# Kernel tuning notes

Hardware: AMD Instinct MI355X
Metric: run time of the kernel (lower is better)

The kernel has to match this reference:

```python
import jax, jax.numpy as jnp
import numpy as np

B, S, E, H = 1, 2048, 512, 8
D = E // H
N = B * S
WIN_HALF = 32  # attention_window 64 -> +/-32
ALPHA = 0.1
LN_EPS = 1e-12
NEG_INF = -1e9


def _build_window_edges():
    # windowed graph: dst i attends to src j with |i-j| <= WIN_HALF, within each batch block
    i = np.arange(S)
    offs = np.arange(-WIN_HALF, WIN_HALF + 1)
    src = i[:, None] + offs[None, :]
    dst = np.broadcast_to(i[:, None], src.shape)
    valid = (src >= 0) & (src < S)
    src, dst = src[valid], dst[valid]
    srcs, dsts = [], []
    for b in range(B):
        srcs.append(src + b * S)
        dsts.append(dst + b * S)
    return (np.concatenate(srcs).astype(np.int32),
            np.concatenate(dsts).astype(np.int32))


def setup_inputs() -> dict:
    key = jax.random.key(0)
    ks = jax.random.split(key, 12)
    sc = 1.0 / np.sqrt(E)
    src_np, dst_np = _build_window_edges()
    return {
        "hidden_states": jax.random.normal(ks[0], (B, S, E), dtype=jnp.float32),
        "attention_mask": jnp.zeros((B, S), dtype=jnp.float32),
        "edge_src": jnp.asarray(src_np),
        "edge_dst": jnp.asarray(dst_np),
        "Wq": jax.random.normal(ks[1], (E, E), dtype=jnp.float32) * sc,
        "bq": jnp.zeros((E,), dtype=jnp.float32),
        "Wk": jax.random.normal(ks[2], (E, E), dtype=jnp.float32) * sc,
        "bk": jnp.zeros((E,), dtype=jnp.float32),
        "Wv": jax.random.normal(ks[3], (E, E), dtype=jnp.float32) * sc,
        "bv": jnp.zeros((E,), dtype=jnp.float32),
        "Wo": jax.random.normal(ks[4], (E, E), dtype=jnp.float32) * sc,
        "bo": jnp.zeros((E,), dtype=jnp.float32),
        "ln_g": jnp.ones((E,), dtype=jnp.float32),
        "ln_b": jnp.zeros((E,), dtype=jnp.float32),
    }


def reference(hidden_states, attention_mask, edge_src, edge_dst,
              Wq, bq, Wk, bk, Wv, bv, Wo, bo, ln_g, ln_b):
    x = hidden_states  # (B,S,E); node ordering n = b*S + s (matches torch reshape)
    q = ((x @ Wq + bq) / jnp.sqrt(jnp.asarray(D, x.dtype))).reshape(N, H, D)
    k = (x @ Wk + bk).reshape(N, H, D)
    v = (x @ Wv + bv).reshape(N, H, D)

    mask = (attention_mask >= 0).reshape(N)  # bool per node

    # u_dot_v('k','q','score'): per-edge, per-head dot product
    score = jnp.einsum('ehd,ehd->eh', k[edge_src], q[edge_dst])  # (Eg,H)
    score = jnp.where(mask[edge_src][:, None], score, NEG_INF)

    # edge_softmax over incoming edges of each destination node
    smax = jax.ops.segment_max(score, edge_dst, num_segments=N)
    p = jnp.exp(score - smax[edge_dst])
    denom = jax.ops.segment_sum(p, edge_dst, num_segments=N)
    p = p / denom[edge_dst]  # (Eg,H)

    # 5 diffusion steps: h <- A h, blended with residual v (dropout off in eval)
    h = v
    for _ in range(5):
        m = h[edge_src] * p[:, :, None]                      # u_mul_e
        h = jax.ops.segment_sum(m, edge_dst, num_segments=N)  # sum('m','h')
        h = (1.0 - ALPHA) * h + ALPHA * v

    attn = h.reshape(B, S, E)

    # DiffuserSelfOutput: dense -> residual add -> LayerNorm
    y = attn @ Wo + bo + hidden_states
    mu = y.mean(-1, keepdims=True)
    var = ((y - mu) ** 2).mean(-1, keepdims=True)
    out = (y - mu) * jax.lax.rsqrt(var + LN_EPS) * ln_g + ln_b
    return out
```

## Files before the change

### kernel.cpp

```cpp
#include <hip/hip_runtime.h>
#include <math.h>

#define S_LEN 2048
#define E_DIM 512
#define NE (S_LEN * E_DIM)
#define H_NUM 8
#define WH 32
#define NOFF 65
#define PROW (H_NUM * NOFF)
#define PN (S_LEN * PROW)

typedef float f32x4 __attribute__((ext_vector_type(4)));
typedef short short8 __attribute__((ext_vector_type(8)));

__device__ __forceinline__ unsigned short f2bf(float f) {
    union { float f; unsigned u; } cv; cv.f = f;
    unsigned u = cv.u;
    u += 0x7fffu + ((u >> 16) & 1u);
    return (unsigned short)(u >> 16);
}
__device__ __forceinline__ unsigned pk2(float x, float y) {
    return (unsigned)f2bf(x) | ((unsigned)f2bf(y) << 16);
}

__device__ __forceinline__ void mfma_gemm_f32(
    const float* __restrict__ A, const float* __restrict__ W,
    const float* __restrict__ bias, float* __restrict__ C,
    float scale, int m0, int n0)
{
    __shared__ unsigned short As[64 * 40];
    __shared__ unsigned short Bs[64 * 40];
    const int tid = threadIdx.x;
    const int lane = tid & 63, wave = tid >> 6;
    const int quad = lane >> 4, l16 = lane & 15;
    const int wr = (wave >> 1) * 32, wc = (wave & 1) * 32;
    const int ar = tid >> 2, ac = (tid & 3) * 8;
    const int bn = tid & 63, bk0 = (tid >> 6) * 8;

    f32x4 acc00 = {0.f,0.f,0.f,0.f}, acc01 = acc00, acc10 = acc00, acc11 = acc00;

    for (int kk = 0; kk < E_DIM; kk += 32) {
        float4 a0 = *(const float4*)(A + (size_t)(m0 + ar) * E_DIM + kk + ac);
        float4 a1 = *(const float4*)(A + (size_t)(m0 + ar) * E_DIM + kk + ac + 4);
        float b[8];
#pragma unroll
        for (int j = 0; j < 8; ++j)
            b[j] = W[(size_t)(kk + bk0 + j) * E_DIM + n0 + bn];
        __syncthreads();
        uint4 ap; ap.x = pk2(a0.x, a0.y); ap.y = pk2(a0.z, a0.w);
        ap.z = pk2(a1.x, a1.y); ap.w = pk2(a1.z, a1.w);
        *(uint4*)(As + ar * 40 + ac) = ap;
        uint4 bp; bp.x = pk2(b[0], b[1]); bp.y = pk2(b[2], b[3]);
        bp.z = pk2(b[4], b[5]); bp.w = pk2(b[6], b[7]);
        *(uint4*)(Bs + bn * 40 + bk0) = bp;
        __syncthreads();
        short8 fa0 = *(const short8*)(As + (wr + l16) * 40 + quad * 8);
        short8 fa1 = *(const short8*)(As + (wr + 16 + l16) * 40 + quad * 8);
        short8 fb0 = *(const short8*)(Bs + (wc + l16) * 40 + quad * 8);
        short8 fb1 = *(const short8*)(Bs + (wc + 16 + l16) * 40 + quad * 8);
        acc00 = __builtin_amdgcn_mfma_f32_16x16x32_bf16(fa0, fb0, acc00, 0, 0, 0);
        acc01 = __builtin_amdgcn_mfma_f32_16x16x32_bf16(fa0, fb1, acc01, 0, 0, 0);
        acc10 = __builtin_amdgcn_mfma_f32_16x16x32_bf16(fa1, fb0, acc10, 0, 0, 0);
        acc11 = __builtin_amdgcn_mfma_f32_16x16x32_bf16(fa1, fb1, acc11, 0, 0, 0);
    }

#pragma unroll
    for (int mi = 0; mi < 2; ++mi) {
#pragma unroll
        for (int ni = 0; ni < 2; ++ni) {
            f32x4 a = (mi == 0) ? ((ni == 0) ? acc00 : acc01)
                                : ((ni == 0) ? acc10 : acc11);
            int n = n0 + wc + ni * 16 + l16;
            float bval = bias[n];
#pragma unroll
            for (int r = 0; r < 4; ++r) {
                int m = m0 + wr + mi * 16 + quad * 4 + r;
                C[(size_t)m * E_DIM + n] = (a[r] + bval) * scale;
            }
        }
    }
}

__global__ __launch_bounds__(256)
void qkv_gemm(const float* __restrict__ x,
              const float* __restrict__ Wq, const float* __restrict__ bq,
              const float* __restrict__ Wk, const float* __restrict__ bk,
              const float* __restrict__ Wv, const float* __restrict__ bv,
              float* __restrict__ q, float* __restrict__ k, float* __restrict__ v)
{
    const float* W; const float* b; float* o; float sc;
    if (blockIdx.z == 0)      { W = Wq; b = bq; o = q; sc = 0.125f; }
    else if (blockIdx.z == 1) { W = Wk; b = bk; o = k; sc = 1.0f; }
    else                      { W = Wv; b = bv; o = v; sc = 1.0f; }
    mfma_gemm_f32(x, W, b, o, sc, blockIdx.y * 64, blockIdx.x * 64);
}

#define SDN 32
__global__ __launch_bounds__(256)
void scores_kernel(const float* __restrict__ q, const float* __restrict__ k,
                   const float* __restrict__ amask, float* __restrict__ P)
{
    const int i0 = blockIdx.x * SDN;
    const int h  = blockIdx.y;
    const int tid = threadIdx.x;
    __shared__ float ks[96 * 68];
    __shared__ float am[96];
    __shared__ float sc[SDN * 66];
    __shared__ float smx[SDN], sidn[SDN];

    for (int e = tid; e < 96 * 16; e += 256) {
        int lr = e >> 4, c4 = e & 15;
        int j = i0 - WH + lr;
        int jc = min(max(j, 0), S_LEN - 1);
        *(float4*)(ks + lr * 68 + c4 * 4) =
            *(const float4*)(k + (size_t)jc * E_DIM + h * 64 + c4 * 4);
    }
    if (tid < 96) {
        int j = i0 - WH + tid;
        am[tid] = (j >= 0 && j < S_LEN) ? amask[j] : -1.0f;
    }

    const int dst = tid >> 3;
    const int og  = tid & 7;
    float4 qreg[16];
    {
        const float4* qrow = (const float4*)(q + (size_t)(i0 + dst) * E_DIM + h * 64);
#pragma unroll
        for (int t = 0; t < 16; ++t) qreg[t] = qrow[t];
    }
    __syncthreads();

    for (int off = og; off < NOFF; off += 8) {
        int j = i0 + dst + off - WH;
        float s;
        if (j < 0 || j >= S_LEN) {
            s = -INFINITY;
        } else {
            int lr = dst + off;
            const float4* kr = (const float4*)(ks + lr * 68);
            float acc = 0.f;
#pragma unroll
            for (int t = 0; t < 16; ++t) {
                float4 a = qreg[t], bb = kr[t];
                acc += a.x * bb.x + a.y * bb.y + a.z * bb.z + a.w * bb.w;
            }
            s = (am[lr] >= 0.f) ? acc : -1e9f;
        }
        sc[dst * 66 + off] = s;
    }
    __syncthreads();

    if (tid < SDN) {
        float mx = -INFINITY;
        for (int o = 0; o < NOFF; ++o) mx = fmaxf(mx, sc[tid * 66 + o]);
        float dn = 0.f;
        for (int o = 0; o < NOFF; ++o) dn += expf(sc[tid * 66 + o] - mx);
        smx[tid] = mx; sidn[tid] = 1.f / dn;
    }
    __syncthreads();

    for (int e = tid; e < SDN * NOFF; e += 256) {
        int d = e / NOFF, off = e - d * NOFF;
        float pv = expf(sc[d * 66 + off] - smx[d]) * sidn[d];
        P[(size_t)(i0 + d) * PROW + h * NOFF + off] = pv;
    }
}

__global__ __launch_bounds__(512)
void diffuse2c(const float* __restrict__ hin, const float* __restrict__ v,
               const float* __restrict__ P, float* __restrict__ hout)
{
    const int i0 = blockIdx.x * 64;
    const int c0 = blockIdx.y * 32;
    const int h  = c0 >> 6;
    const int tid = threadIdx.x;
    __shared__ float hs[192 * 36];
    __shared__ float h1[128 * 36];
    __shared__ float ps[128 * NOFF];

    for (int e = tid; e < 192 * 8; e += 512) {
        int lr = e >> 3, c4 = e & 7;
        int j = i0 - 64 + lr;
        int jc = min(max(j, 0), S_LEN - 1);
        *(float4*)(hs + lr * 36 + c4 * 4) =
            *(const float4*)(hin + (size_t)jc * E_DIM + c0 + c4 * 4);
    }
    for (int e = tid; e < 128 * NOFF; e += 512) {
        int mr = e / NOFF, o = e - mr * NOFF;
        int j = i0 - 32 + mr;
        int jc = min(max(j, 0), S_LEN - 1);
        ps[e] = P[(size_t)jc * PROW + h * NOFF + o];
    }
    __syncthreads();

    const int ci = tid & 7;
    const int g  = tid >> 3;

    {
        float4 a0 = {0,0,0,0}, a1 = a0;
        const int mb = g * 2;
        for (int lr = 0; lr < 66; ++lr) {
            float4 hval = *(const float4*)(hs + (mb + lr) * 36 + ci * 4);
            if (lr <= 64) {
                float p = ps[mb * NOFF + lr];
                a0.x += p * hval.x; a0.y += p * hval.y; a0.z += p * hval.z; a0.w += p * hval.w;
            }
            int o1 = lr - 1;
            if ((unsigned)o1 <= 64u) {
                float p = ps[(mb + 1) * NOFF + o1];
                a1.x += p * hval.x; a1.y += p * hval.y; a1.z += p * hval.z; a1.w += p * hval.w;
            }
        }
#pragma unroll
        for (int r = 0; r < 2; ++r) {
            float4 a = r ? a1 : a0;
            int j = i0 - 32 + mb + r;
            int jc = min(max(j, 0), S_LEN - 1);
            float4 vv = *(const float4*)(v + (size_t)jc * E_DIM + c0 + ci * 4);
            float4 o;
            o.x = 0.9f * a.x + 0.1f * vv.x;
            o.y = 0.9f * a.y + 0.1f * vv.y;
            o.z = 0.9f * a.z + 0.1f * vv.z;
            o.w = 0.9f * a.w + 0.1f * vv.w;
            *(float4*)(h1 + (mb + r) * 36 + ci * 4) = o;
        }
    }
    __syncthreads();

    {
        float4 a = {0,0,0,0};
        for (int off = 0; off < NOFF; ++off) {
            float4 hval = *(const float4*)(h1 + (g + off) * 36 + ci * 4);
            float p = ps[(g + 32) * NOFF + off];
            a.x += p * hval.x; a.y += p * hval.y; a.z += p * hval.z; a.w += p * hval.w;
        }
        size_t base = (size_t)(i0 + g) * E_DIM + c0 + ci * 4;
        float4 vv = *(const float4*)(v + base);
        float4 o;
        o.x = 0.9f * a.x + 0.1f * vv.x;
        o.y = 0.9f * a.y + 0.1f * vv.y;
        o.z = 0.9f * a.z + 0.1f * vv.z;
        o.w = 0.9f * a.w + 0.1f * vv.w;
        *(float4*)(hout + base) = o;
    }
}

__global__ __launch_bounds__(512)
void oln2(const float* __restrict__ hB, const float* __restrict__ v,
          const float* __restrict__ P, const float* __restrict__ Wo,
          const float* __restrict__ bo, const float* __restrict__ x,
          const float* __restrict__ g, const float* __restrict__ lb,
          float* __restrict__ out)
{
    __shared__ unsigned short As[16 * 40];
    __shared__ unsigned short Bs[512 * 40];
    __shared__ float hBs[80 * 37];
    __shared__ float Ps[16 * PROW];
    __shared__ float vs[16 * 32];
    __shared__ float rsum[8][16], rsq[8][16];
    const int tid = threadIdx.x;
    const int lane = tid & 63, wave = tid >> 6;
    const int quad = lane >> 4, l16 = lane & 15;
    const int m0 = blockIdx.x * 16;
    const int n = tid;

    for (int e = tid; e < 16 * PROW; e += 512)
        Ps[e] = P[(size_t)(m0 + e / PROW) * PROW + (e % PROW)];

    f32x4 acc[4];
#pragma unroll
    for (int t = 0; t < 4; ++t) acc[t] = (f32x4){0.f,0.f,0.f,0.f};

    for (int kk = 0; kk < E_DIM; kk += 32) {
        const int hd = kk >> 6;
        float4 hv4;
        {
            int lr = tid >> 3, c4 = tid & 7;
            int j = m0 - 32 + lr;
            int jc = min(max(j, 0), S_LEN - 1);
            hv4 = *(const float4*)(hB + (size_t)jc * E_DIM + kk + c4 * 4);
        }
        float4 hv4b;
        if (tid < 128) {
            int lr = 64 + (tid >> 3), c4 = tid & 7;
            int j = m0 - 32 + lr;
            int jc = min(max(j, 0), S_LEN - 1);
            hv4b = *(const float4*)(hB + (size_t)jc * E_DIM + kk + c4 * 4);
        }
        float4 vv4;
        if (tid < 128)
            vv4 = *(const float4*)(v + (size_t)(m0 + (tid >> 3)) * E_DIM + kk + (tid & 7) * 4);
        float bcol[32];
#pragma unroll
        for (int j = 0; j < 32; ++j)
            bcol[j] = Wo[(size_t)(kk + j) * E_DIM + n];

        __syncthreads();
        {
            int lr = tid >> 3, c4 = tid & 7;
            *(float4*)(hBs + lr * 37 + c4 * 4) = hv4;
        }
        if (tid < 128) {
            int lr = 64 + (tid >> 3), c4 = tid & 7;
            *(float4*)(hBs + lr * 37 + c4 * 4) = hv4b;
        }
        if (tid < 128)
            *(float4*)(vs + (tid >> 3) * 32 + (tid & 7) * 4) = vv4;
#pragma unroll
        for (int t = 0; t < 4; ++t) {
            uint4 bp;
            bp.x = pk2(bcol[t*8+0], bcol[t*8+1]); bp.y = pk2(bcol[t*8+2], bcol[t*8+3]);
            bp.z = pk2(bcol[t*8+4], bcol[t*8+5]); bp.w = pk2(bcol[t*8+6], bcol[t*8+7]);
            *(uint4*)(Bs + n * 40 + t * 8) = bp;
        }
        __syncthreads();

        if (tid < 256) {
            int r = tid >> 4, cp = (tid & 15) * 2;
            const float* pr = Ps + r * PROW + hd * NOFF;
            float a0 = 0.f, a1 = 0.f;
            for (int off = 0; off < NOFF; ++off) {
                float p = pr[off];
                a0 += p * hBs[(r + off) * 37 + cp];
                a1 += p * hBs[(r + off) * 37 + cp + 1];
            }
            float h0 = 0.9f * a0 + 0.1f * vs[r * 32 + cp];
            float h1 = 0.9f * a1 + 0.1f * vs[r * 32 + cp + 1];
            *(unsigned*)(As + r * 40 + cp) = pk2(h0, h1);
        }
        __syncthreads();

        short8 fa = *(const short8*)(As + l16 * 40 + quad * 8);
#pragma unroll
        for (int nt = 0; nt < 4; ++nt) {
            short8 fb = *(const short8*)(Bs + (wave * 64 + nt * 16 + l16) * 40 + quad * 8);
            acc[nt] = __builtin_amdgcn_mfma_f32_16x16x32_bf16(fa, fb, acc[nt], 0, 0, 0);
        }
    }

    float s[4] = {0.f,0.f,0.f,0.f}, s2[4] = {0.f,0.f,0.f,0.f};
#pragma unroll
    for (int nt = 0; nt < 4; ++nt) {
        int nc = wave * 64 + nt * 16 + l16;
        float bv = bo[nc];
#pragma unroll
        for (int r = 0; r < 4; ++r) {
            int m = m0 + quad * 4 + r;
            float vl = acc[nt][r] + bv + x[(size_t)m * E_DIM + nc];
            acc[nt][r] = vl;
            s[r] += vl; s2[r] += vl * vl;
        }
    }
#pragma unroll
    for (int o = 1; o < 16; o <<= 1) {
#pragma unroll
        for (int r = 0; r < 4; ++r) {
            s[r]  += __shfl_xor(s[r], o, 64);
            s2[r] += __shfl_xor(s2[r], o, 64);
        }
    }
    if (l16 == 0) {
#pragma unroll
        for (int r = 0; r < 4; ++r) {
            rsum[wave][quad * 4 + r] = s[r];
            rsq[wave][quad * 4 + r]  = s2[r];
        }
    }
    __syncthreads();
    float mu[4], rs[4];
#pragma unroll
    for (int r = 0; r < 4; ++r) {
        int rl = quad * 4 + r;
        float tot = 0.f, tot2 = 0.f;
#pragma unroll
        for (int w = 0; w < 8; ++w) { tot += rsum[w][rl]; tot2 += rsq[w][rl]; }
        float m_ = tot * (1.f / 512.f);
        float var = tot2 * (1.f / 512.f) - m_ * m_;
        mu[r] = m_; rs[r] = rsqrtf(var + 1e-12f);
    }
#pragma unroll
    for (int nt = 0; nt < 4; ++nt) {
        int nc = wave * 64 + nt * 16 + l16;
        float gv = g[nc], bbv = lb[nc];
#pragma unroll
        for (int r = 0; r < 4; ++r) {
            int m = m0 + quad * 4 + r;
            out[(size_t)m * E_DIM + nc] = (acc[nt][r] - mu[r]) * rs[r] * gv + bbv;
        }
    }
}

extern "C" void kernel_launch(void* const* d_in, const int* in_sizes, int n_in,
                              void* d_out, int out_size, void* d_ws, size_t ws_size,
                              hipStream_t stream)
{
    const float* x     = (const float*)d_in[0];
    const float* amask = (const float*)d_in[1];
    const float* Wq = (const float*)d_in[4];
    const float* bq = (const float*)d_in[5];
    const float* Wk = (const float*)d_in[6];
    const float* bk = (const float*)d_in[7];
    const float* Wv = (const float*)d_in[8];
    const float* bv = (const float*)d_in[9];
    const float* Wo = (const float*)d_in[10];
    const float* bo = (const float*)d_in[11];
    const float* lng = (const float*)d_in[12];
    const float* lnb = (const float*)d_in[13];
    float* out = (float*)d_out;

    float* ws = (float*)d_ws;
    float* q  = ws;
    float* k  = ws + (size_t)NE;
    float* v  = ws + (size_t)2 * NE;
    float* P  = ws + (size_t)3 * NE;
    float* hA = ws + (size_t)3 * NE + PN;
    float* hB = hA + (size_t)NE;

    qkv_gemm<<<dim3(8, 32, 3), 256, 0, stream>>>(x, Wq, bq, Wk, bk, Wv, bv, q, k, v);

    scores_kernel<<<dim3(64, 8), 256, 0, stream>>>(q, k, amask, P);

    diffuse2c<<<dim3(32, 16), 512, 0, stream>>>(v,  v, P, hA);
    diffuse2c<<<dim3(32, 16), 512, 0, stream>>>(hA, v, P, hB);

    oln2<<<128, 512, 0, stream>>>(hB, v, P, Wo, bo, x, lng, lnb, out);
}
```

Measured before the change: 186.2 us.

## Fuse first diffusion step into scores kernel and simplify output GEMM

The first diffusion step (P·v blended with v) now runs inside the scores kernel, reusing the freshly computed probabilities in shared memory and reloading v into the k tile buffer. The two diffuse2c launches then cover steps two to five, and the output projection kernel no longer computes the final diffusion step inside its GEMM k-loop. This removes the serialized per-k-iteration diffusion work and an extra barrier from the low-occupancy output kernel. In exchange, the scores kernel gets more work and shared memory.

After: 174.9 us. -6.1%, faster.

```diff
diff --git a/kernel.cpp b/kernel.cpp
--- a/kernel.cpp
+++ b/kernel.cpp
@@ -97,8 +97,9 @@
 
 #define SDN 32
 __global__ __launch_bounds__(256)
-void scores_kernel(const float* __restrict__ q, const float* __restrict__ k,
-                   const float* __restrict__ amask, float* __restrict__ P)
+void scores_d1(const float* __restrict__ q, const float* __restrict__ k,
+               const float* __restrict__ v, const float* __restrict__ amask,
+               float* __restrict__ P, float* __restrict__ hA)
 {
     const int i0 = blockIdx.x * SDN;
     const int h  = blockIdx.y;
@@ -107,6 +108,7 @@
     __shared__ float am[96];
     __shared__ float sc[SDN * 66];
     __shared__ float smx[SDN], sidn[SDN];
+    __shared__ float ps[SDN * NOFF];
 
     for (int e = tid; e < 96 * 16; e += 256) {
         int lr = e >> 4, c4 = e & 15;
@@ -150,6 +152,13 @@
     }
     __syncthreads();
 
+    for (int e = tid; e < 96 * 16; e += 256) {
+        int lr = e >> 4, c4 = e & 15;
+        int j = i0 - WH + lr;
+        int jc = min(max(j, 0), S_LEN - 1);
+        *(float4*)(ks + lr * 68 + c4 * 4) =
+            *(const float4*)(v + (size_t)jc * E_DIM + h * 64 + c4 * 4);
+    }
     if (tid < SDN) {
         float mx = -INFINITY;
         for (int o = 0; o < NOFF; ++o) mx = fmaxf(mx, sc[tid * 66 + o]);
@@ -163,6 +172,38 @@
         int d = e / NOFF, off = e - d * NOFF;
         float pv = expf(sc[d * 66 + off] - smx[d]) * sidn[d];
         P[(size_t)(i0 + d) * PROW + h * NOFF + off] = pv;
+        ps[e] = pv;
+    }
+    __syncthreads();
+
+    {
+        const int ci = tid & 15;
+        const int ob = (tid >> 4) * 2;
+        float4 a0 = {0,0,0,0}, a1 = a0;
+        for (int lr = ob; lr < ob + 66; ++lr) {
+            float4 hval = *(const float4*)(ks + lr * 68 + ci * 4);
+            int o0 = lr - ob;
+            if (o0 <= 64) {
+                float p = ps[ob * NOFF + o0];
+                a0.x += p * hval.x; a0.y += p * hval.y; a0.z += p * hval.z; a0.w += p * hval.w;
+            }
+            int o1 = o0 - 1;
+            if ((unsigned)o1 <= 64u) {
+                float p = ps[(ob + 1) * NOFF + o1];
+                a1.x += p * hval.x; a1.y += p * hval.y; a1.z += p * hval.z; a1.w += p * hval.w;
+            }
+        }
+#pragma unroll
+        for (int r = 0; r < 2; ++r) {
+            float4 a = r ? a1 : a0;
+            float4 vv = *(const float4*)(ks + (WH + ob + r) * 68 + ci * 4);
+            float4 o;
+            o.x = 0.9f * a.x + 0.1f * vv.x;
+            o.y = 0.9f * a.y + 0.1f * vv.y;
+            o.z = 0.9f * a.z + 0.1f * vv.z;
+            o.w = 0.9f * a.w + 0.1f * vv.w;
+            *(float4*)(hA + (size_t)(i0 + ob + r) * E_DIM + h * 64 + ci * 4) = o;
+        }
     }
 }
 
@@ -246,17 +287,13 @@
 }
 
 __global__ __launch_bounds__(512)
-void oln2(const float* __restrict__ hB, const float* __restrict__ v,
-          const float* __restrict__ P, const float* __restrict__ Wo,
-          const float* __restrict__ bo, const float* __restrict__ x,
-          const float* __restrict__ g, const float* __restrict__ lb,
-          float* __restrict__ out)
+void oln(const float* __restrict__ hsrc, const float* __restrict__ Wo,
+         const float* __restrict__ bo, const float* __restrict__ x,
+         const float* __restrict__ g, const float* __restrict__ lb,
+         float* __restrict__ out)
 {
     __shared__ unsigned short As[16 * 40];
     __shared__ unsigned short Bs[512 * 40];
-    __shared__ float hBs[80 * 37];
-    __shared__ float Ps[16 * PROW];
-    __shared__ float vs[16 * 32];
     __shared__ float rsum[8][16], rsq[8][16];
     const int tid = threadIdx.x;
     const int lane = tid & 63, wave = tid >> 6;
@@ -264,48 +301,23 @@
     const int m0 = blockIdx.x * 16;
     const int n = tid;
 
-    for (int e = tid; e < 16 * PROW; e += 512)
-        Ps[e] = P[(size_t)(m0 + e / PROW) * PROW + (e % PROW)];
-
     f32x4 acc[4];
 #pragma unroll
     for (int t = 0; t < 4; ++t) acc[t] = (f32x4){0.f,0.f,0.f,0.f};
 
     for (int kk = 0; kk < E_DIM; kk += 32) {
-        const int hd = kk >> 6;
-        float4 hv4;
-        {
-            int lr = tid >> 3, c4 = tid & 7;
-            int j = m0 - 32 + lr;
-            int jc = min(max(j, 0), S_LEN - 1);
-            hv4 = *(const float4*)(hB + (size_t)jc * E_DIM + kk + c4 * 4);
-        }
-        float4 hv4b;
-        if (tid < 128) {
-            int lr = 64 + (tid >> 3), c4 = tid & 7;
-            int j = m0 - 32 + lr;
-            int jc = min(max(j, 0), S_LEN - 1);
-            hv4b = *(const float4*)(hB + (size_t)jc * E_DIM + kk + c4 * 4);
-        }
-        float4 vv4;
+        float4 av;
         if (tid < 128)
-            vv4 = *(const float4*)(v + (size_t)(m0 + (tid >> 3)) * E_DIM + kk + (tid & 7) * 4);
+            av = *(const float4*)(hsrc + (size_t)(m0 + (tid >> 3)) * E_DIM + kk + (tid & 7) * 4);
         float bcol[32];
 #pragma unroll
         for (int j = 0; j < 32; ++j)
             bcol[j] = Wo[(size_t)(kk + j) * E_DIM + n];
-
         __syncthreads();
-        {
-            int lr = tid >> 3, c4 = tid & 7;
-            *(float4*)(hBs + lr * 37 + c4 * 4) = hv4;
-        }
         if (tid < 128) {
-            int lr = 64 + (tid >> 3), c4 = tid & 7;
-            *(float4*)(hBs + lr * 37 + c4 * 4) = hv4b;
-        }
-        if (tid < 128)
-            *(float4*)(vs + (tid >> 3) * 32 + (tid & 7) * 4) = vv4;
+            uint2 ap; ap.x = pk2(av.x, av.y); ap.y = pk2(av.z, av.w);
+            *(uint2*)(As + (tid >> 3) * 40 + (tid & 7) * 4) = ap;
+        }
 #pragma unroll
         for (int t = 0; t < 4; ++t) {
             uint4 bp;
@@ -314,22 +326,6 @@
             *(uint4*)(Bs + n * 40 + t * 8) = bp;
         }
         __syncthreads();
-
-        if (tid < 256) {
-            int r = tid >> 4, cp = (tid & 15) * 2;
-            const float* pr = Ps + r * PROW + hd * NOFF;
-            float a0 = 0.f, a1 = 0.f;
-            for (int off = 0; off < NOFF; ++off) {
-                float p = pr[off];
-                a0 += p * hBs[(r + off) * 37 + cp];
-                a1 += p * hBs[(r + off) * 37 + cp + 1];
-            }
-            float h0 = 0.9f * a0 + 0.1f * vs[r * 32 + cp];
-            float h1 = 0.9f * a1 + 0.1f * vs[r * 32 + cp + 1];
-            *(unsigned*)(As + r * 40 + cp) = pk2(h0, h1);
-        }
-        __syncthreads();
-
         short8 fa = *(const short8*)(As + l16 * 40 + quad * 8);
 #pragma unroll
         for (int nt = 0; nt < 4; ++nt) {
@@ -418,10 +414,10 @@
 
     qkv_gemm<<<dim3(8, 32, 3), 256, 0, stream>>>(x, Wq, bq, Wk, bk, Wv, bv, q, k, v);
 
-    scores_kernel<<<dim3(64, 8), 256, 0, stream>>>(q, k, amask, P);
-
-    diffuse2c<<<dim3(32, 16), 512, 0, stream>>>(v,  v, P, hA);
+    scores_d1<<<dim3(64, 8), 256, 0, stream>>>(q, k, v, amask, P, hA);
+
     diffuse2c<<<dim3(32, 16), 512, 0, stream>>>(hA, v, P, hB);
-
-    oln2<<<128, 512, 0, stream>>>(hB, v, P, Wo, bo, x, lng, lnb, out);
-}
+    diffuse2c<<<dim3(32, 16), 512, 0, stream>>>(hB, v, P, hA);
+
+    oln<<<128, 512, 0, stream>>>(hA, Wo, bo, x, lng, lnb, out);
+}
```
